# Kernel tuning notes

Hardware: AMD Instinct MI355X
Metric: run time of the kernel (lower is better)

The kernel has to match this reference:

```python
import jax, jax.numpy as jnp
import numpy as np

# Model hyperparameters (match init_kwargs / module defaults)
B, P, F_IN, H, K, OUT = 1024, 256, 8, 16, 8, 1


def _lin_init(key, out_f, in_f, bias=True):
    # torch nn.Linear default: U(-1/sqrt(in), 1/sqrt(in))
    kw, kb = jax.random.split(key)
    bound = 1.0 / np.sqrt(in_f)
    W = jax.random.uniform(kw, (out_f, in_f), jnp.float32, -bound, bound)
    if bias:
        b = jax.random.uniform(kb, (out_f,), jnp.float32, -bound, bound)
        return W, b
    return W


def setup_inputs() -> dict:
    key = jax.random.key(0)
    ks = jax.random.split(key, 7)
    x = jax.random.normal(ks[0], (B, P * F_IN), jnp.float32)
    W1 = _lin_init(ks[1], H, F_IN, bias=False)          # part_encode[0], bias=False
    W2, b2 = _lin_init(ks[2], H, H)                      # part_encode[2]
    W3, b3 = _lin_init(ks[3], H, H)                      # part_encode[4]
    We, be = _lin_init(ks[4], H, 2 * H)                  # edge MLP Linear(2H, H)
    Wo1, bo1 = _lin_init(ks[5], H // 2, H)               # output[0]
    Wo2, bo2 = _lin_init(ks[6], OUT, H // 2)             # output[2]
    return {"x": x, "W1": W1, "W2": W2, "b2": b2, "W3": W3, "b3": b3,
            "We": We, "be": be, "Wo1": Wo1, "bo1": bo1, "Wo2": Wo2, "bo2": bo2}


def reference(x, W1, W2, b2, W3, b3, We, be, Wo1, bo1, Wo2, bo2):
    b = x.shape[0]
    # part_encode MLP on flattened particles
    h = x.reshape(b * P, F_IN)
    h = jax.nn.elu(h @ W1.T)
    h = jax.nn.elu(h @ W2.T + b2)
    h = jax.nn.elu(h @ W3.T + b3)
    h = h.reshape(b, P, H)                               # [B,P,H]

    # Dynamic kNN graph per batch element (knn includes self at distance 0,
    # matching torch_cluster.knn on identical query/source sets)
    sq = jnp.sum(h * h, axis=-1)                         # [B,P]
    dist = sq[:, :, None] + sq[:, None, :] - 2.0 * jnp.einsum('bid,bjd->bij', h, h)
    _, idx = jax.lax.top_k(-dist, K)                     # [B,P,K] nearest neighbors

    # Gather neighbor features per graph
    xj = jax.vmap(lambda hb, ib: hb[ib])(h, idx)         # [B,P,K,H]
    xi = jnp.broadcast_to(h[:, :, None, :], xj.shape)    # [B,P,K,H]
    edge = jnp.concatenate([xi, xj - xi], axis=-1)       # [B,P,K,2H]

    # Edge MLP + max aggregation (EdgeConv message nn([x_i, x_j - x_i]), aggr='max')
    m = jax.nn.elu(edge @ We.T + be)                     # [B,P,K,H]
    node = jnp.max(m, axis=2)                            # [B,P,H]

    # avg_pool_x over nodes of each graph
    pooled = jnp.mean(node, axis=1)                      # [B,H]

    # output MLP + sigmoid (act_out=True, batchnorm=False)
    o = jax.nn.elu(pooled @ Wo1.T + bo1)
    o = o @ Wo2.T + bo2
    return jax.nn.sigmoid(o)                             # [B,OUT]
```

## Files before the change

kernel.cpp:

```cpp
#include <hip/hip_runtime.h>
#include <math.h>

#define NB 1024
#define NP 256
#define FIN 8
#define NH 16
#define NK 8

#define REP8A(X)  X(0) X(1) X(2) X(3) X(4) X(5) X(6) X(7)
#define REP16A(X) X(0) X(1) X(2) X(3) X(4) X(5) X(6) X(7) X(8) X(9) X(10) X(11) X(12) X(13) X(14) X(15)
#define REP16B(X) X(0) X(1) X(2) X(3) X(4) X(5) X(6) X(7) X(8) X(9) X(10) X(11) X(12) X(13) X(14) X(15)

typedef short s8v __attribute__((ext_vector_type(8)));
typedef float f4v __attribute__((ext_vector_type(4)));
typedef unsigned int u4v __attribute__((ext_vector_type(4)));

__device__ __forceinline__ float elu_f(float v) {
    return v > 0.f ? v : (__expf(v) - 1.f);
}
__device__ __forceinline__ unsigned bf16r(float f) {
    unsigned u = __float_as_uint(f);
    return (u + 0x7FFFu + ((u >> 16) & 1u)) >> 16;
}
__device__ __forceinline__ float ush2f(unsigned short u) {
    return __uint_as_float(((unsigned)u) << 16);
}

#define CE(a, b) { float lo_ = fminf(a, b), hi_ = fmaxf(a, b); a = lo_; b = hi_; }
#define SORT8(x0,x1,x2,x3,x4,x5,x6,x7) \
    CE(x0,x1) CE(x2,x3) CE(x4,x5) CE(x6,x7) \
    CE(x0,x2) CE(x1,x3) CE(x4,x6) CE(x5,x7) \
    CE(x1,x2) CE(x5,x6) \
    CE(x0,x4) CE(x1,x5) CE(x2,x6) CE(x3,x7) \
    CE(x2,x4) CE(x3,x5) \
    CE(x1,x2) CE(x3,x4) CE(x5,x6)
#define MERGE8(x0,x1,x2,x3,x4,x5,x6,x7) \
    R0 = fminf(R0, x7); R1 = fminf(R1, x6); R2 = fminf(R2, x5); R3 = fminf(R3, x4); \
    R4 = fminf(R4, x3); R5 = fminf(R5, x2); R6 = fminf(R6, x1); R7 = fminf(R7, x0); \
    CE(R0,R4) CE(R1,R5) CE(R2,R6) CE(R3,R7) \
    CE(R0,R2) CE(R1,R3) CE(R4,R6) CE(R5,R7) \
    CE(R0,R1) CE(R2,R3) CE(R4,R5) CE(R6,R7)

#define KEYV(val, c) __uint_as_float((__float_as_uint((val) + sqp2) & 0xFFFFFF00u) | (unsigned)(c))

#define KNN_TT(ttc) { \
    const s8v af = *(const s8v*)&hF[4 * w + (ttc)][lq][lc * 8]; \
    float R0, R1, R2, R3, R4, R5, R6, R7; \
    R0=R1=R2=R3=R4=R5=R6=R7 = __uint_as_float(0x7F7FFFFFu); \
    for (int jt2 = 0; jt2 < 8; ++jt2) { \
        const s8v b1a = *(const s8v*)&hF[2 * jt2][lq][lc * 8]; \
        const s8v b1b = *(const s8v*)&hF[2 * jt2 + 1][lq][lc * 8]; \
        const s8v b2a = __builtin_shufflevector(b1a, b1a, 4, 5, 6, 7, 0, 1, 2, 3); \
        const s8v b2b = __builtin_shufflevector(b1b, b1b, 4, 5, 6, 7, 0, 1, 2, 3); \
        const float4 sqa = *(const float4*)&sq2arr[32 * jt2 + 4 * lq]; \
        const float4 sqb = *(const float4*)&sq2arr[32 * jt2 + 16 + 4 * lq]; \
        f4v z = {0.f, 0.f, 0.f, 0.f}; \
        f4v a1 = __builtin_amdgcn_mfma_f32_16x16x32_bf16(b1a, af, z, 0, 0, 0); \
        f4v a2 = __builtin_amdgcn_mfma_f32_16x16x32_bf16(b2a, af, z, 0, 0, 0); \
        f4v a3 = __builtin_amdgcn_mfma_f32_16x16x32_bf16(b1b, af, z, 0, 0, 0); \
        f4v a4 = __builtin_amdgcn_mfma_f32_16x16x32_bf16(b2b, af, z, 0, 0, 0); \
        const int c0 = 32 * jt2 + 4 * lq, c1 = c0 + 16; \
        float k0 = KEYV(sqa.x - a1[0] - a2[0], c0 + 0); \
        float k1 = KEYV(sqa.y - a1[1] - a2[1], c0 + 1); \
        float k2 = KEYV(sqa.z - a1[2] - a2[2], c0 + 2); \
        float k3 = KEYV(sqa.w - a1[3] - a2[3], c0 + 3); \
        float k4 = KEYV(sqb.x - a3[0] - a4[0], c1 + 0); \
        float k5 = KEYV(sqb.y - a3[1] - a4[1], c1 + 1); \
        float k6 = KEYV(sqb.z - a3[2] - a4[2], c1 + 2); \
        float k7 = KEYV(sqb.w - a3[3] - a4[3], c1 + 3); \
        SORT8(k0, k1, k2, k3, k4, k5, k6, k7) \
        MERGE8(k0, k1, k2, k3, k4, k5, k6, k7) \
    } \
    { float o0 = __shfl_xor(R0, 16), o1 = __shfl_xor(R1, 16), \
            o2 = __shfl_xor(R2, 16), o3 = __shfl_xor(R3, 16), \
            o4 = __shfl_xor(R4, 16), o5 = __shfl_xor(R5, 16), \
            o6 = __shfl_xor(R6, 16), o7 = __shfl_xor(R7, 16); \
      MERGE8(o0, o1, o2, o3, o4, o5, o6, o7) } \
    { float o0 = __shfl_xor(R0, 32), o1 = __shfl_xor(R1, 32), \
            o2 = __shfl_xor(R2, 32), o3 = __shfl_xor(R3, 32), \
            o4 = __shfl_xor(R4, 32), o5 = __shfl_xor(R5, 32), \
            o6 = __shfl_xor(R6, 32), o7 = __shfl_xor(R7, 32); \
      MERGE8(o0, o1, o2, o3, o4, o5, o6, o7) } \
    if (lq == (ttc)) { \
        unsigned plo = (__float_as_uint(R0) & 0xFFu) \
                     | ((__float_as_uint(R1) & 0xFFu) << 8) \
                     | ((__float_as_uint(R2) & 0xFFu) << 16) \
                     | ((__float_as_uint(R3) & 0xFFu) << 24); \
        unsigned phi = (__float_as_uint(R4) & 0xFFu) \
                     | ((__float_as_uint(R5) & 0xFFu) << 8) \
                     | ((__float_as_uint(R6) & 0xFFu) << 16) \
                     | ((__float_as_uint(R7) & 0xFFu) << 24); \
        jjarr[w][16 * (ttc) + lc] = make_uint2(plo, phi); \
    } \
}

__global__ __attribute__((amdgpu_flat_work_group_size(256, 256),
                          amdgpu_waves_per_eu(2, 4)))
void edgenet_kernel(
    const float* __restrict__ gx,
    const float* __restrict__ gW1, const float* __restrict__ gW2, const float* __restrict__ gb2,
    const float* __restrict__ gW3, const float* __restrict__ gb3,
    const float* __restrict__ gWe, const float* __restrict__ gbe,
    const float* __restrict__ gWo1, const float* __restrict__ gbo1,
    const float* __restrict__ gWo2, const float* __restrict__ gbo2,
    float* __restrict__ gout)
{
    const int b  = blockIdx.x;
    const int t  = threadIdx.x;
    const int w  = t >> 6;
    const int lq = (t >> 4) & 3;
    const int lc = t & 15;

    __shared__ __align__(16) unsigned short hF[16][4][136];
    __shared__ __align__(16) float sq2arr[256];
    __shared__ __align__(16) float sbaseA[4][64][17];
    __shared__ __align__(16) uint2 jjarr[4][64];
    __shared__ float spool[64];

    float xi0, xi1, xi2, xi3, xi4, xi5, xi6, xi7;
    {
        const float4* xr = reinterpret_cast<const float4*>(gx + (size_t)b * (NP * FIN) + t * FIN);
        float4 v0 = xr[0], v1 = xr[1];
        xi0 = v0.x; xi1 = v0.y; xi2 = v0.z; xi3 = v0.w;
        xi4 = v1.x; xi5 = v1.y; xi6 = v1.z; xi7 = v1.w;
    }

    float l1_0,l1_1,l1_2,l1_3,l1_4,l1_5,l1_6,l1_7,l1_8,l1_9,l1_10,l1_11,l1_12,l1_13,l1_14,l1_15;
    float l2_0,l2_1,l2_2,l2_3,l2_4,l2_5,l2_6,l2_7,l2_8,l2_9,l2_10,l2_11,l2_12,l2_13,l2_14,l2_15;
    float hp0,hp1,hp2,hp3,hp4,hp5,hp6,hp7,hp8,hp9,hp10,hp11,hp12,hp13,hp14,hp15;

#define L1_BODY(i) s = fmaf(gW1[(o_) * FIN + i], xi##i, s);
#define L1_O(o) { const int o_ = (o); float s = 0.f; REP8A(L1_BODY) l1_##o = elu_f(s); }
    REP16A(L1_O)
#undef L1_O
#undef L1_BODY
#define L2_BODY(i) s = fmaf(gW2[(o_) * NH + i], l1_##i, s);
#define L2_O(o) { const int o_ = (o); float s = gb2[o_]; REP16B(L2_BODY) l2_##o = elu_f(s); }
    REP16A(L2_O)
#undef L2_O
#undef L2_BODY
#define L3_BODY(i) s = fmaf(gW3[(o_) * NH + i], l2_##i, s);
#define L3_O(o) { const int o_ = (o); float s = gb3[o_]; REP16B(L3_BODY) hp##o = elu_f(s); }
    REP16A(L3_O)
#undef L3_O
#undef L3_BODY

    {
        float* sb = &sbaseA[w][t & 63][0];
#define BAS_BODY(i) s = fmaf(gWe[(o_) * 32 + i] - gWe[(o_) * 32 + 16 + i], hp##i, s);
#define BAS_O(o) { const int o_ = (o); float s = gbe[o_]; REP16B(BAS_BODY) sb[o_] = s; }
        REP16A(BAS_O)
#undef BAS_O
#undef BAS_BODY
    }

    s8v eB1;
    {
        float4 wv = *reinterpret_cast<const float4*>(gWe + lc * 32 + 16 + 4 * lq);
        unsigned h0 = bf16r(wv.x), h1 = bf16r(wv.y), h2 = bf16r(wv.z), h3 = bf16r(wv.w);
        unsigned g0 = bf16r(wv.x - ush2f((unsigned short)h0));
        unsigned g1 = bf16r(wv.y - ush2f((unsigned short)h1));
        unsigned g2 = bf16r(wv.z - ush2f((unsigned short)h2));
        unsigned g3 = bf16r(wv.w - ush2f((unsigned short)h3));
        eB1 = (s8v){(short)h0, (short)h1, (short)h2, (short)h3,
                    (short)g0, (short)g1, (short)g2, (short)g3};
    }

    float sqp = 0.f;
#define SQ_I(i) sqp = fmaf(hp##i, hp##i, sqp);
    REP16A(SQ_I)
#undef SQ_I
    const float sqp2 = 0.5f * sqp;

#define PACKQ(q, A, B, C, D) { \
    unsigned ha = bf16r(hp##A), hb = bf16r(hp##B), hc = bf16r(hp##C), hd = bf16r(hp##D); \
    float ra = hp##A - ush2f((unsigned short)ha); \
    float rb = hp##B - ush2f((unsigned short)hb); \
    float rc = hp##C - ush2f((unsigned short)hc); \
    float rd = hp##D - ush2f((unsigned short)hd); \
    unsigned la = bf16r(ra), lb = bf16r(rb), lcc = bf16r(rc), ld = bf16r(rd); \
    u4v pk; pk.x = ha | (hb << 16); pk.y = hc | (hd << 16); \
            pk.z = la | (lb << 16); pk.w = lcc | (ld << 16); \
    *(u4v*)&hF[t >> 4][q][(t & 15) * 8] = pk; }
    PACKQ(0, 0, 1, 2, 3)
    PACKQ(1, 4, 5, 6, 7)
    PACKQ(2, 8, 9, 10, 11)
    PACKQ(3, 12, 13, 14, 15)
#undef PACKQ
    sq2arr[t] = sqp2;
    __syncthreads();

    KNN_TT(0)
    KNN_TT(1)
    KNN_TT(2)
    KNN_TT(3)

    float psum = 0.f;
    {
        const s8v eB2 = __builtin_shufflevector(eB1, eB1, 4, 5, 6, 7, 0, 1, 2, 3);
        const int erow = lc;
        #pragma unroll 4
        for (int tt = 0; tt < 32; ++tt) {
            uint2 jv = jjarr[w][2 * tt + (erow >> 3)];
            unsigned word = (erow & 4) ? jv.y : jv.x;
            int jp = (int)((word >> ((erow & 3) * 8)) & 0xFFu);
            const s8v av = *(const s8v*)&hF[jp >> 4][lq][(jp & 15) * 8];
            f4v z = {0.f, 0.f, 0.f, 0.f};
            f4v d1 = __builtin_amdgcn_mfma_f32_16x16x32_bf16(av, eB1, z, 0, 0, 0);
            d1     = __builtin_amdgcn_mfma_f32_16x16x32_bf16(av, eB2, d1, 0, 0, 0);
            float mx = fmaxf(fmaxf(d1[0], d1[1]), fmaxf(d1[2], d1[3]));
            mx = fmaxf(mx, __shfl_xor(mx, 16, 64));
            float bz = sbaseA[w][2 * tt + (lq >> 1)][lc];
            psum += elu_f(mx + bz);
        }
    }
    psum += __shfl_xor(psum, 16, 64);
    psum += __shfl_xor(psum, 32, 64);
    if ((t & 63) < 16) spool[(w << 4) + lc] = psum;
    __syncthreads();

    if (t == 0) {
#define PL(i) const float pl##i = (spool[i] + spool[16 + i] + spool[32 + i] + spool[48 + i]) * (1.f / 512.f);
        REP16A(PL)
#undef PL
        float o1_0,o1_1,o1_2,o1_3,o1_4,o1_5,o1_6,o1_7;
#define HD_BODY(i) s = fmaf(gWo1[(o_) * NH + i], pl##i, s);
#define HD_O(o) { const int o_ = (o); float s = gbo1[o_]; REP16B(HD_BODY) o1_##o = elu_f(s); }
        REP8A(HD_O)
#undef HD_O
#undef HD_BODY
        float o2 = gbo2[0];
        o2 = fmaf(gWo2[0], o1_0, o2); o2 = fmaf(gWo2[1], o1_1, o2);
        o2 = fmaf(gWo2[2], o1_2, o2); o2 = fmaf(gWo2[3], o1_3, o2);
        o2 = fmaf(gWo2[4], o1_4, o2); o2 = fmaf(gWo2[5], o1_5, o2);
        o2 = fmaf(gWo2[6], o1_6, o2); o2 = fmaf(gWo2[7], o1_7, o2);
        gout[b] = 1.f / (1.f + expf(-o2));
    }
}

extern "C" void kernel_launch(void* const* d_in, const int* in_sizes, int n_in,
                              void* d_out, int out_size, void* d_ws, size_t ws_size,
                              hipStream_t stream) {
    const float* x   = (const float*)d_in[0];
    const float* W1  = (const float*)d_in[1];
    const float* W2  = (const float*)d_in[2];
    const float* b2  = (const float*)d_in[3];
    const float* W3  = (const float*)d_in[4];
    const float* b3  = (const float*)d_in[5];
    const float* We  = (const float*)d_in[6];
    const float* be  = (const float*)d_in[7];
    const float* Wo1 = (const float*)d_in[8];
    const float* bo1 = (const float*)d_in[9];
    const float* Wo2 = (const float*)d_in[10];
    const float* bo2 = (const float*)d_in[11];
    float* out = (float*)d_out;

    hipLaunchKernelGGL(edgenet_kernel, dim3(NB), dim3(NP), 0, stream,
                       x, W1, W2, b2, W3, b3, We, be, Wo1, bo1, Wo2, bo2, out);
}
```

Measured before the change: 131.5 us.

## Interleave four kNN query tiles per column sweep and fold distance terms into MFMA

```diff
diff --git a/kernel.cpp b/kernel.cpp
--- a/kernel.cpp
+++ b/kernel.cpp
@@ -34,65 +34,14 @@
     CE(x0,x4) CE(x1,x5) CE(x2,x6) CE(x3,x7) \
     CE(x2,x4) CE(x3,x5) \
     CE(x1,x2) CE(x3,x4) CE(x5,x6)
-#define MERGE8(x0,x1,x2,x3,x4,x5,x6,x7) \
-    R0 = fminf(R0, x7); R1 = fminf(R1, x6); R2 = fminf(R2, x5); R3 = fminf(R3, x4); \
-    R4 = fminf(R4, x3); R5 = fminf(R5, x2); R6 = fminf(R6, x1); R7 = fminf(R7, x0); \
-    CE(R0,R4) CE(R1,R5) CE(R2,R6) CE(R3,R7) \
-    CE(R0,R2) CE(R1,R3) CE(R4,R6) CE(R5,R7) \
-    CE(R0,R1) CE(R2,R3) CE(R4,R5) CE(R6,R7)
+#define MERGE8P(P,x0,x1,x2,x3,x4,x5,x6,x7) \
+    P##0 = fminf(P##0, x7); P##1 = fminf(P##1, x6); P##2 = fminf(P##2, x5); P##3 = fminf(P##3, x4); \
+    P##4 = fminf(P##4, x3); P##5 = fminf(P##5, x2); P##6 = fminf(P##6, x1); P##7 = fminf(P##7, x0); \
+    CE(P##0,P##4) CE(P##1,P##5) CE(P##2,P##6) CE(P##3,P##7) \
+    CE(P##0,P##2) CE(P##1,P##3) CE(P##4,P##6) CE(P##5,P##7) \
+    CE(P##0,P##1) CE(P##2,P##3) CE(P##4,P##5) CE(P##6,P##7)
 
 #define KEYV(val, c) __uint_as_float((__float_as_uint((val) + sqp2) & 0xFFFFFF00u) | (unsigned)(c))
-
-#define KNN_TT(ttc) { \
-    const s8v af = *(const s8v*)&hF[4 * w + (ttc)][lq][lc * 8]; \
-    float R0, R1, R2, R3, R4, R5, R6, R7; \
-    R0=R1=R2=R3=R4=R5=R6=R7 = __uint_as_float(0x7F7FFFFFu); \
-    for (int jt2 = 0; jt2 < 8; ++jt2) { \
-        const s8v b1a = *(const s8v*)&hF[2 * jt2][lq][lc * 8]; \
-        const s8v b1b = *(const s8v*)&hF[2 * jt2 + 1][lq][lc * 8]; \
-        const s8v b2a = __builtin_shufflevector(b1a, b1a, 4, 5, 6, 7, 0, 1, 2, 3); \
-        const s8v b2b = __builtin_shufflevector(b1b, b1b, 4, 5, 6, 7, 0, 1, 2, 3); \
-        const float4 sqa = *(const float4*)&sq2arr[32 * jt2 + 4 * lq]; \
-        const float4 sqb = *(const float4*)&sq2arr[32 * jt2 + 16 + 4 * lq]; \
-        f4v z = {0.f, 0.f, 0.f, 0.f}; \
-        f4v a1 = __builtin_amdgcn_mfma_f32_16x16x32_bf16(b1a, af, z, 0, 0, 0); \
-        f4v a2 = __builtin_amdgcn_mfma_f32_16x16x32_bf16(b2a, af, z, 0, 0, 0); \
-        f4v a3 = __builtin_amdgcn_mfma_f32_16x16x32_bf16(b1b, af, z, 0, 0, 0); \
-        f4v a4 = __builtin_amdgcn_mfma_f32_16x16x32_bf16(b2b, af, z, 0, 0, 0); \
-        const int c0 = 32 * jt2 + 4 * lq, c1 = c0 + 16; \
-        float k0 = KEYV(sqa.x - a1[0] - a2[0], c0 + 0); \
-        float k1 = KEYV(sqa.y - a1[1] - a2[1], c0 + 1); \
-        float k2 = KEYV(sqa.z - a1[2] - a2[2], c0 + 2); \
-        float k3 = KEYV(sqa.w - a1[3] - a2[3], c0 + 3); \
-        float k4 = KEYV(sqb.x - a3[0] - a4[0], c1 + 0); \
-        float k5 = KEYV(sqb.y - a3[1] - a4[1], c1 + 1); \
-        float k6 = KEYV(sqb.z - a3[2] - a4[2], c1 + 2); \
-        float k7 = KEYV(sqb.w - a3[3] - a4[3], c1 + 3); \
-        SORT8(k0, k1, k2, k3, k4, k5, k6, k7) \
-        MERGE8(k0, k1, k2, k3, k4, k5, k6, k7) \
-    } \
-    { float o0 = __shfl_xor(R0, 16), o1 = __shfl_xor(R1, 16), \
-            o2 = __shfl_xor(R2, 16), o3 = __shfl_xor(R3, 16), \
-            o4 = __shfl_xor(R4, 16), o5 = __shfl_xor(R5, 16), \
-            o6 = __shfl_xor(R6, 16), o7 = __shfl_xor(R7, 16); \
-      MERGE8(o0, o1, o2, o3, o4, o5, o6, o7) } \
-    { float o0 = __shfl_xor(R0, 32), o1 = __shfl_xor(R1, 32), \
-            o2 = __shfl_xor(R2, 32), o3 = __shfl_xor(R3, 32), \
-            o4 = __shfl_xor(R4, 32), o5 = __shfl_xor(R5, 32), \
-            o6 = __shfl_xor(R6, 32), o7 = __shfl_xor(R7, 32); \
-      MERGE8(o0, o1, o2, o3, o4, o5, o6, o7) } \
-    if (lq == (ttc)) { \
-        unsigned plo = (__float_as_uint(R0) & 0xFFu) \
-                     | ((__float_as_uint(R1) & 0xFFu) << 8) \
-                     | ((__float_as_uint(R2) & 0xFFu) << 16) \
-                     | ((__float_as_uint(R3) & 0xFFu) << 24); \
-        unsigned phi = (__float_as_uint(R4) & 0xFFu) \
-                     | ((__float_as_uint(R5) & 0xFFu) << 8) \
-                     | ((__float_as_uint(R6) & 0xFFu) << 16) \
-                     | ((__float_as_uint(R7) & 0xFFu) << 24); \
-        jjarr[w][16 * (ttc) + lc] = make_uint2(plo, phi); \
-    } \
-}
 
 __global__ __attribute__((amdgpu_flat_work_group_size(256, 256),
                           amdgpu_waves_per_eu(2, 4)))
@@ -190,10 +139,79 @@
     sq2arr[t] = sqp2;
     __syncthreads();
 
-    KNN_TT(0)
-    KNN_TT(1)
-    KNN_TT(2)
-    KNN_TT(3)
+#define LDNAF(i) s8v naf##i; { \
+    u4v au = __builtin_bit_cast(u4v, *(const s8v*)&hF[4 * w + (i)][lq][lc * 8]); \
+    au.x ^= 0x80008000u; au.y ^= 0x80008000u; au.z ^= 0x80008000u; au.w ^= 0x80008000u; \
+    naf##i = __builtin_bit_cast(s8v, au); }
+    LDNAF(0) LDNAF(1) LDNAF(2) LDNAF(3)
+#undef LDNAF
+
+    float Ra0,Ra1,Ra2,Ra3,Ra4,Ra5,Ra6,Ra7;
+    float Rb0,Rb1,Rb2,Rb3,Rb4,Rb5,Rb6,Rb7;
+    float Rc0,Rc1,Rc2,Rc3,Rc4,Rc5,Rc6,Rc7;
+    float Rd0,Rd1,Rd2,Rd3,Rd4,Rd5,Rd6,Rd7;
+    {
+        const float big = __uint_as_float(0x7F7FFFFFu);
+        Ra0=Ra1=Ra2=Ra3=Ra4=Ra5=Ra6=Ra7 = big;
+        Rb0=Rb1=Rb2=Rb3=Rb4=Rb5=Rb6=Rb7 = big;
+        Rc0=Rc1=Rc2=Rc3=Rc4=Rc5=Rc6=Rc7 = big;
+        Rd0=Rd1=Rd2=Rd3=Rd4=Rd5=Rd6=Rd7 = big;
+    }
+
+    for (int jt2 = 0; jt2 < 8; ++jt2) {
+        const s8v b1a = *(const s8v*)&hF[2 * jt2][lq][lc * 8];
+        const s8v b1b = *(const s8v*)&hF[2 * jt2 + 1][lq][lc * 8];
+        const s8v b2a = __builtin_shufflevector(b1a, b1a, 4, 5, 6, 7, 0, 1, 2, 3);
+        const s8v b2b = __builtin_shufflevector(b1b, b1b, 4, 5, 6, 7, 0, 1, 2, 3);
+        const f4v sqa = *(const f4v*)&sq2arr[32 * jt2 + 4 * lq];
+        const f4v sqb = *(const f4v*)&sq2arr[32 * jt2 + 16 + 4 * lq];
+        const int c0 = 32 * jt2 + 4 * lq, c1 = c0 + 16;
+
+#define GTT(naf, P) { \
+        f4v da = __builtin_amdgcn_mfma_f32_16x16x32_bf16(b1a, naf, sqa, 0, 0, 0); \
+        da     = __builtin_amdgcn_mfma_f32_16x16x32_bf16(b2a, naf, da,  0, 0, 0); \
+        f4v db = __builtin_amdgcn_mfma_f32_16x16x32_bf16(b1b, naf, sqb, 0, 0, 0); \
+        db     = __builtin_amdgcn_mfma_f32_16x16x32_bf16(b2b, naf, db,  0, 0, 0); \
+        float k0 = KEYV(da[0], c0 + 0), k1 = KEYV(da[1], c0 + 1); \
+        float k2 = KEYV(da[2], c0 + 2), k3 = KEYV(da[3], c0 + 3); \
+        float k4 = KEYV(db[0], c1 + 0), k5 = KEYV(db[1], c1 + 1); \
+        float k6 = KEYV(db[2], c1 + 2), k7 = KEYV(db[3], c1 + 3); \
+        SORT8(k0, k1, k2, k3, k4, k5, k6, k7) \
+        MERGE8P(P, k0, k1, k2, k3, k4, k5, k6, k7) }
+        GTT(naf0, Ra)
+        GTT(naf1, Rb)
+        GTT(naf2, Rc)
+        GTT(naf3, Rd)
+#undef GTT
+    }
+
+#define FIN_TT(P, ttc) { \
+    { float o0 = __shfl_xor(P##0, 16), o1 = __shfl_xor(P##1, 16), \
+            o2 = __shfl_xor(P##2, 16), o3 = __shfl_xor(P##3, 16), \
+            o4 = __shfl_xor(P##4, 16), o5 = __shfl_xor(P##5, 16), \
+            o6 = __shfl_xor(P##6, 16), o7 = __shfl_xor(P##7, 16); \
+      MERGE8P(P, o0, o1, o2, o3, o4, o5, o6, o7) } \
+    { float o0 = __shfl_xor(P##0, 32), o1 = __shfl_xor(P##1, 32), \
+            o2 = __shfl_xor(P##2, 32), o3 = __shfl_xor(P##3, 32), \
+            o4 = __shfl_xor(P##4, 32), o5 = __shfl_xor(P##5, 32), \
+            o6 = __shfl_xor(P##6, 32), o7 = __shfl_xor(P##7, 32); \
+      MERGE8P(P, o0, o1, o2, o3, o4, o5, o6, o7) } \
+    if (lq == (ttc)) { \
+        unsigned plo = (__float_as_uint(P##0) & 0xFFu) \
+                     | ((__float_as_uint(P##1) & 0xFFu) << 8) \
+                     | ((__float_as_uint(P##2) & 0xFFu) << 16) \
+                     | ((__float_as_uint(P##3) & 0xFFu) << 24); \
+        unsigned phi = (__float_as_uint(P##4) & 0xFFu) \
+                     | ((__float_as_uint(P##5) & 0xFFu) << 8) \
+                     | ((__float_as_uint(P##6) & 0xFFu) << 16) \
+                     | ((__float_as_uint(P##7) & 0xFFu) << 24); \
+        jjarr[w][16 * (ttc) + lc] = make_uint2(plo, phi); \
+    } }
+    FIN_TT(Ra, 0)
+    FIN_TT(Rb, 1)
+    FIN_TT(Rc, 2)
+    FIN_TT(Rd, 3)
+#undef FIN_TT
 
     float psum = 0.f;
     {
```

After: 125.8 us. -4.3%, faster.
